# Kernel tuning notes

Measured on AMD Instinct MI355X. Metric: run time of the kernel, lower is better.

The kernel has to match this reference:

```python
import jax, jax.numpy as jnp
import numpy as np

# dims (see shape_source): emb_dim=256, input_size=256 -> d_model=1024
B, L = 8, 1024
QUES = 4000
EMB = 256
DM = 1024          # input_size + 768
DI = 2048          # expand * d_model
N = 16             # d_state
DTR = 64           # dt_rank = ceil(d_model/16)
K = 4              # d_conv
EPS = 1e-12


def setup_inputs() -> dict:
    key = jax.random.key(0)
    ks = jax.random.split(key, 16)
    s = 0.02
    nrm = lambda k, sh: jax.random.normal(k, sh, dtype=jnp.float32) * s
    return {
        "x": jax.random.randint(ks[0], (B, L), 0, 2 * QUES + 1),
        "q_id": jax.random.randint(ks[1], (B, L), 0, QUES),
        "emb_table": nrm(ks[2], (2 * QUES + 1, EMB)),
        "ques_cont": nrm(ks[3], (QUES, 768)),
        "ln0_g": jnp.ones((DM,), jnp.float32),
        "ln0_b": jnp.zeros((DM,), jnp.float32),
        "in_proj_w": nrm(ks[4], (2 * DI, DM)),
        "conv_w": nrm(ks[5], (DI, K)),
        "conv_b": jnp.zeros((DI,), jnp.float32),
        "x_proj_w": nrm(ks[6], (DTR + 2 * N, DI)),
        "dt_proj_w": nrm(ks[7], (DI, DTR)),
        "dt_proj_b": nrm(ks[8], (DI,)),
        "A_log": jnp.log(jax.random.uniform(ks[9], (DI, N), jnp.float32, 1.0, 16.0)),
        "D_param": jnp.ones((DI,), jnp.float32),
        "out_proj_w": nrm(ks[10], (DM, DI)),
        "ln1_g": jnp.ones((DM,), jnp.float32),
        "ln1_b": jnp.zeros((DM,), jnp.float32),
        "fc_w": nrm(ks[11], (QUES, DM)),
        "fc_b": jnp.zeros((QUES,), jnp.float32),
    }


def _ln(x, g, b):
    m = x.mean(-1, keepdims=True)
    v = ((x - m) ** 2).mean(-1, keepdims=True)
    return (x - m) / jnp.sqrt(v + EPS) * g + b


def _mamba(xm, in_proj_w, conv_w, conv_b, x_proj_w, dt_proj_w, dt_proj_b,
           A_log, D_param, out_proj_w):
    # xm: [B, L, DM]
    u_r = xm @ in_proj_w.T                           # [B, L, 2*DI]
    u, r = jnp.split(u_r, 2, axis=-1)                # each [B, L, DI]
    Lq = u.shape[1]
    # causal depthwise conv1d (padding=K-1, truncated to L)
    u_pad = jnp.pad(u, ((0, 0), (K - 1, 0), (0, 0)))
    conv = sum(u_pad[:, k:k + Lq, :] * conv_w[:, k] for k in range(K)) + conv_b
    u = jax.nn.silu(conv)
    dbl = u @ x_proj_w.T                             # [B, L, DTR+2N]
    dt, Bm, Cm = dbl[..., :DTR], dbl[..., DTR:DTR + N], dbl[..., DTR + N:]
    delta = jax.nn.softplus(dt @ dt_proj_w.T + dt_proj_b)   # [B, L, DI]
    A = -jnp.exp(A_log)                              # [DI, N]

    def step(h, ins):
        d_t, b_t, c_t, u_t = ins                     # [B,DI],[B,N],[B,N],[B,DI]
        dA = jnp.exp(d_t[:, :, None] * A)            # [B, DI, N]
        h = dA * h + d_t[:, :, None] * b_t[:, None, :] * u_t[:, :, None]
        y_t = jnp.einsum('bdn,bn->bd', h, c_t)
        return h, y_t

    xs = (delta.transpose(1, 0, 2), Bm.transpose(1, 0, 2),
          Cm.transpose(1, 0, 2), u.transpose(1, 0, 2))
    h0 = jnp.zeros((u.shape[0], DI, N), u.dtype)
    _, ys = jax.lax.scan(step, h0, xs)               # ys: [L, B, DI]
    y = ys.transpose(1, 0, 2) + u * D_param
    y = y * jax.nn.silu(r)
    return y @ out_proj_w.T                          # [B, L, DM]


def reference(x, q_id, emb_table, ques_cont, ln0_g, ln0_b, in_proj_w, conv_w,
              conv_b, x_proj_w, dt_proj_w, dt_proj_b, A_log, D_param,
              out_proj_w, ln1_g, ln1_b, fc_w, fc_b):
    x_e = emb_table[x]                               # [B, L, 256]
    x_c = ques_cont[q_id]                            # [B, L, 768]
    item = _ln(jnp.concatenate([x_e, x_c], axis=-1), ln0_g, ln0_b)
    # source loop applies every layer to item_emb; only the last layer's
    # output is used, so compute exactly that one layer (num_layers=2 branch).
    h = _mamba(item, in_proj_w, conv_w, conv_b, x_proj_w, dt_proj_w,
               dt_proj_b, A_log, D_param, out_proj_w)
    out = _ln(h + item, ln1_g, ln1_b)
    return jax.nn.sigmoid(out @ fc_w.T + fc_b)       # [B, L, QUES]
```

## Files before the change

kernel.cpp:

```cpp
#include <hip/hip_runtime.h>
#include <cstdint>
#include <cstddef>

#define L_SEQ 1024
#define BATCH 8
#define DMODEL 1024
#define DINNER 2048
#define NSTATE 16
#define DTRANK 64
#define NQ 4000
#define NROWS (BATCH * L_SEQ)
#define CH 32
#define NCH (L_SEQ / CH)

typedef float f32x4 __attribute__((ext_vector_type(4)));
typedef __bf16 bf16x8 __attribute__((ext_vector_type(8)));

#define AS1 __attribute__((address_space(1)))
#define AS3 __attribute__((address_space(3)))

__device__ __forceinline__ unsigned short f2bf(float f) {
  union { float f; unsigned int u; } c; c.f = f;
  unsigned int u = c.u;
  unsigned int r = u + 0x7fffu + ((u >> 16) & 1u);
  return (unsigned short)(r >> 16);
}

__device__ __forceinline__ float sigmoidf_(float x) { return 1.f / (1.f + expf(-x)); }

__global__ void cast_bf16_k(const float* __restrict__ src, unsigned short* __restrict__ dst, int n) {
  int i = blockIdx.x * blockDim.x + threadIdx.x;
  if (i < n) dst[i] = f2bf(src[i]);
}

__device__ __forceinline__ float blk_sum(float v, float* s) {
  #pragma unroll
  for (int o = 32; o > 0; o >>= 1) v += __shfl_down(v, o, 64);
  int w = threadIdx.x >> 6;
  if ((threadIdx.x & 63) == 0) s[w] = v;
  __syncthreads();
  float r = s[0] + s[1] + s[2] + s[3];
  __syncthreads();
  return r;
}

__global__ __launch_bounds__(256) void embed_ln0_k(
    const int* __restrict__ x, const int* __restrict__ qid,
    const float* __restrict__ emb, const float* __restrict__ qc,
    const float* __restrict__ g, const float* __restrict__ bta,
    float* __restrict__ item, unsigned short* __restrict__ item_bf)
{
  __shared__ float sbuf[4];
  int i = blockIdx.x;
  int t = threadIdx.x;
  float4 v;
  if (t < 64) v = *(const float4*)&emb[(size_t)x[i] * 256 + t * 4];
  else        v = *(const float4*)&qc[(size_t)qid[i] * 768 + t * 4 - 256];
  float tot = blk_sum(v.x + v.y + v.z + v.w, sbuf);
  float mean = tot * (1.f / 1024.f);
  float dx = v.x - mean, dy = v.y - mean, dz = v.z - mean, dw = v.w - mean;
  float var = blk_sum(dx*dx + dy*dy + dz*dz + dw*dw, sbuf) * (1.f / 1024.f);
  float rstd = rsqrtf(var + 1e-12f);
  float vals[4] = {dx, dy, dz, dw};
  size_t rb = (size_t)i * 1024;
  #pragma unroll
  for (int j = 0; j < 4; j++) {
    int c = t * 4 + j;
    float o = vals[j] * rstd * g[c] + bta[c];
    item[rb + c] = o;
    item_bf[rb + c] = f2bf(o);
  }
}

template <int EPI>
__global__ __launch_bounds__(256) void gemm_bt_k(
    const unsigned short* __restrict__ A, const unsigned short* __restrict__ Bw,
    float* __restrict__ C, const float* __restrict__ bias,
    unsigned short* __restrict__ aux,
    int M, int N, int K)
{
  __shared__ __align__(16) unsigned short As[128 * 64];
  __shared__ __align__(16) unsigned short Bs[128 * 64];
  const int tid = threadIdx.x;
  const int m0 = blockIdx.x * 128;
  const int n0 = blockIdx.y * 128;
  const int w = tid >> 6, lane = tid & 63;
  const int wrow = (w >> 1) * 64, wcol = (w & 1) * 64;
  const int quad = lane >> 4, lid = lane & 15;

  const int srow = lane >> 3;
  const int schunk = (lane & 7) ^ srow;

  const unsigned short* Abase = A + (size_t)(m0 + w * 8 + srow) * K + schunk * 8;
  const unsigned short* Bbase[4];
  #pragma unroll
  for (int i = 0; i < 4; i++) {
    int rB = n0 + w * 8 + i * 32 + srow;
    if (rB > N - 1) rB = N - 1;
    Bbase[i] = Bw + (size_t)rB * K + schunk * 8;
  }

  f32x4 acc[4][4] = {};

  for (int k0 = 0; k0 < K; k0 += 64) {
    #pragma unroll
    for (int i = 0; i < 4; i++) {
      int rA = w * 8 + i * 32;
      __builtin_amdgcn_global_load_lds(
          (const AS1 unsigned int*)(Abase + (size_t)i * 32 * K + k0),
          (AS3 unsigned int*)&As[rA * 64], 16, 0, 0);
      __builtin_amdgcn_global_load_lds(
          (const AS1 unsigned int*)(Bbase[i] + k0),
          (AS3 unsigned int*)&Bs[rA * 64], 16, 0, 0);
    }
    __syncthreads();
    #pragma unroll
    for (int kk = 0; kk < 64; kk += 32) {
      bf16x8 af[4], bfr[4];
      #pragma unroll
      for (int mi = 0; mi < 4; mi++) {
        int r = wrow + mi * 16 + lid;
        int slot = ((kk >> 3) + quad) ^ (lid & 7);
        af[mi] = *(const bf16x8*)&As[r * 64 + slot * 8];
      }
      #pragma unroll
      for (int ni = 0; ni < 4; ni++) {
        int r = wcol + ni * 16 + lid;
        int slot = ((kk >> 3) + quad) ^ (lid & 7);
        bfr[ni] = *(const bf16x8*)&Bs[r * 64 + slot * 8];
      }
      #pragma unroll
      for (int mi = 0; mi < 4; mi++)
        #pragma unroll
        for (int ni = 0; ni < 4; ni++)
          acc[mi][ni] = __builtin_amdgcn_mfma_f32_16x16x32_bf16(af[mi], bfr[ni], acc[mi][ni], 0, 0, 0);
    }
    __syncthreads();
  }

  #pragma unroll
  for (int mi = 0; mi < 4; mi++) {
    #pragma unroll
    for (int ni = 0; ni < 4; ni++) {
      int col = n0 + wcol + ni * 16 + lid;
      if (col >= N) continue;
      #pragma unroll
      for (int r = 0; r < 4; r++) {
        int row = m0 + wrow + mi * 16 + quad * 4 + r;
        float v = acc[mi][ni][r];
        if (EPI == 1) v = sigmoidf_(v + bias[col]);
        if (EPI == 2) { float xx = v + bias[col]; v = fmaxf(xx, 0.f) + log1pf(expf(-fabsf(xx))); }
        C[(size_t)row * N + col] = v;
        if (EPI == 3 && col < 64) aux[(size_t)row * 64 + col] = f2bf(v);
      }
    }
  }
}

template <int EPI>
__global__ __launch_bounds__(512, 2) void gemm256_k(
    const unsigned short* __restrict__ A, const unsigned short* __restrict__ Bw,
    float* __restrict__ C, const float* __restrict__ bias,
    int M, int N, int K)
{
  __shared__ __align__(16) unsigned short As[2][256 * 64];
  __shared__ __align__(16) unsigned short Bs[2][256 * 64];
  const int tid = threadIdx.x;

  const int gx = gridDim.x;
  const int nwg = gx * gridDim.y;
  int bid = blockIdx.y * gx + blockIdx.x;
  if ((nwg & 7) == 0) bid = (bid & 7) * (nwg >> 3) + (bid >> 3);
  const int m0 = (bid % gx) * 256;
  const int n0 = (bid / gx) * 256;

  const int w = tid >> 6, lane = tid & 63;
  const int wrow = (w >> 2) * 128;
  const int wcol = (w & 3) * 64;
  const int quad = lane >> 4, lid = lane & 15;

  const int srow = lane >> 3;
  const int schunk = (lane & 7) ^ srow;

  const unsigned short* Ab = A + (size_t)(m0 + w * 8 + srow) * K + schunk * 8;
  const unsigned short* Bb[4];
  #pragma unroll
  for (int i = 0; i < 4; i++) {
    int rB = n0 + w * 8 + i * 64 + srow;
    if (rB > N - 1) rB = N - 1;
    Bb[i] = Bw + (size_t)rB * K + schunk * 8;
  }

  f32x4 acc[8][4] = {};

  auto stage = [&](int buf, int k0) {
    #pragma unroll
    for (int i = 0; i < 4; i++) {
      int rg = (i * 64 + w * 8) * 64;
      __builtin_amdgcn_global_load_lds(
          (const AS1 unsigned int*)(Ab + (size_t)i * 64 * K + k0),
          (AS3 unsigned int*)&As[buf][rg], 16, 0, 0);
      __builtin_amdgcn_global_load_lds(
          (const AS1 unsigned int*)(Bb[i] + k0),
          (AS3 unsigned int*)&Bs[buf][rg], 16, 0, 0);
    }
  };

  const int nt = K >> 6;
  stage(0, 0);
  __syncthreads();

  for (int kt = 0; kt < nt; ++kt) {
    const int cur = kt & 1;
    if (kt + 1 < nt) stage(cur ^ 1, (kt + 1) << 6);

    bf16x8 bfr[4][2];
    #pragma unroll
    for (int ni = 0; ni < 4; ni++) {
      #pragma unroll
      for (int kk2 = 0; kk2 < 2; kk2++) {
        int r = wcol + ni * 16 + lid;
        int slot = (kk2 * 4 + quad) ^ (lid & 7);
        bfr[ni][kk2] = *(const bf16x8*)&Bs[cur][r * 64 + slot * 8];
      }
    }
    #pragma unroll
    for (int mi = 0; mi < 8; mi++) {
      bf16x8 af[2];
      #pragma unroll
      for (int kk2 = 0; kk2 < 2; kk2++) {
        int r = wrow + mi * 16 + lid;
        int slot = (kk2 * 4 + quad) ^ (lid & 7);
        af[kk2] = *(const bf16x8*)&As[cur][r * 64 + slot * 8];
      }
      #pragma unroll
      for (int ni = 0; ni < 4; ni++) {
        acc[mi][ni] = __builtin_amdgcn_mfma_f32_16x16x32_bf16(af[0], bfr[ni][0], acc[mi][ni], 0, 0, 0);
        acc[mi][ni] = __builtin_amdgcn_mfma_f32_16x16x32_bf16(af[1], bfr[ni][1], acc[mi][ni], 0, 0, 0);
      }
    }
    __syncthreads();
  }

  #pragma unroll
  for (int mi = 0; mi < 8; mi++) {
    #pragma unroll
    for (int ni = 0; ni < 4; ni++) {
      int col = n0 + wcol + ni * 16 + lid;
      if (col >= N) continue;
      #pragma unroll
      for (int r = 0; r < 4; r++) {
        int row = m0 + wrow + mi * 16 + quad * 4 + r;
        float v = acc[mi][ni][r];
        if (EPI == 1) v = sigmoidf_(v + bias[col]);
        C[(size_t)row * N + col] = v;
      }
    }
  }
}

__global__ void conv_silu_k(const float* __restrict__ u_r, const float* __restrict__ w,
                            const float* __restrict__ cb, float* __restrict__ uc,
                            unsigned short* __restrict__ uc_bf)
{
  int idx = blockIdx.x * blockDim.x + threadIdx.x;
  if (idx >= BATCH * L_SEQ * DINNER) return;
  int d = idx & (DINNER - 1);
  int l = (idx >> 11) & (L_SEQ - 1);
  int b = idx >> 21;
  float4 wv = ((const float4*)w)[d];
  size_t rb = ((size_t)b * L_SEQ + l) * (2 * DINNER) + d;
  float acc = cb[d];
  acc += wv.w * u_r[rb];
  if (l >= 1) acc += wv.z * u_r[rb - (2 * DINNER)];
  if (l >= 2) acc += wv.y * u_r[rb - 2 * (2 * DINNER)];
  if (l >= 3) acc += wv.x * u_r[rb - 3 * (2 * DINNER)];
  float s = acc * sigmoidf_(acc);
  uc[idx] = s;
  uc_bf[idx] = f2bf(s);
}

__global__ void a2_k(const float* __restrict__ Alog, float* __restrict__ a2t)
{
  int i = blockIdx.x * blockDim.x + threadIdx.x;
  if (i >= DINNER * NSTATE) return;
  int d = i >> 4, n = i & 15;
  a2t[n * DINNER + d] = -expf(Alog[i]) * 1.4426950408889634f;
}

__global__ __launch_bounds__(64) void scan1_k(
    const float* __restrict__ dlt, const float* __restrict__ uc,
    const float* __restrict__ dbl, const float* __restrict__ a2t,
    float* __restrict__ Pbuf, float* __restrict__ Qbuf)
{
  int c = blockIdx.x;
  int dg = blockIdx.y;
  int b = blockIdx.z;
  int d = dg * 64 + threadIdx.x;
  float a2[NSTATE], P[NSTATE], q[NSTATE];
  #pragma unroll
  for (int n = 0; n < NSTATE; n++) {
    a2[n] = a2t[n * DINNER + d];
    P[n] = 1.f; q[n] = 0.f;
  }
  size_t base = ((size_t)(b * L_SEQ + c * CH)) * DINNER + d;
  const float* bc = dbl + (size_t)(b * L_SEQ + c * CH) * 96 + 64;
  for (int t = 0; t < CH; t++) {
    float dl = dlt[base];
    float du = dl * uc[base];
    #pragma unroll
    for (int n = 0; n < NSTATE; n++) {
      float dA = exp2f(dl * a2[n]);
      q[n] = dA * q[n] + du * bc[n];
      P[n] *= dA;
    }
    base += DINNER;
    bc += 96;
  }
  size_t ob = ((size_t)((b * NCH + c) * NSTATE)) * DINNER + d;
  #pragma unroll
  for (int n = 0; n < NSTATE; n++) {
    Pbuf[ob + (size_t)n * DINNER] = P[n];
    Qbuf[ob + (size_t)n * DINNER] = q[n];
  }
}

__global__ void scan_carry_k(const float* __restrict__ Pbuf, float* __restrict__ Qbuf)
{
  int idx = blockIdx.x * blockDim.x + threadIdx.x;
  if (idx >= BATCH * NSTATE * DINNER) return;
  int d = idx & (DINNER - 1);
  int n = (idx >> 11) & 15;
  int b = idx >> 15;
  float h = 0.f;
  for (int c = 0; c < NCH; c++) {
    size_t o = ((size_t)((b * NCH + c) * NSTATE + n)) * DINNER + d;
    float P = Pbuf[o];
    float q = Qbuf[o];
    Qbuf[o] = h;
    h = P * h + q;
  }
}

__global__ __launch_bounds__(64) void scan2_k(
    const float* __restrict__ dlt, const float* __restrict__ uc,
    const float* __restrict__ dbl, const float* __restrict__ a2t,
    const float* __restrict__ Qbuf, const float* __restrict__ u_r,
    const float* __restrict__ Dp, unsigned short* __restrict__ ybf)
{
  int c = blockIdx.x;
  int dg = blockIdx.y;
  int b = blockIdx.z;
  int d = dg * 64 + threadIdx.x;
  float a2[NSTATE], h[NSTATE];
  size_t ob = ((size_t)((b * NCH + c) * NSTATE)) * DINNER + d;
  #pragma unroll
  for (int n = 0; n < NSTATE; n++) {
    a2[n] = a2t[n * DINNER + d];
    h[n] = Qbuf[ob + (size_t)n * DINNER];
  }
  float Dd = Dp[d];
  size_t base = ((size_t)(b * L_SEQ + c * CH)) * DINNER + d;
  const float* bc = dbl + (size_t)(b * L_SEQ + c * CH) * 96 + 64;
  const float* rp = u_r + (size_t)(b * L_SEQ + c * CH) * (2 * DINNER) + DINNER + d;
  for (int t = 0; t < CH; t++) {
    float dl = dlt[base];
    float uval = uc[base];
    float du = dl * uval;
    float yv = 0.f;
    #pragma unroll
    for (int n = 0; n < NSTATE; n++) {
      float dA = exp2f(dl * a2[n]);
      h[n] = dA * h[n] + du * bc[n];
      yv += h[n] * bc[NSTATE + n];
    }
    float rv = *rp;
    float val = (yv + uval * Dd) * (rv * sigmoidf_(rv));
    ybf[base] = f2bf(val);
    base += DINNER;
    bc += 96;
    rp += 2 * DINNER;
  }
}

__global__ __launch_bounds__(256) void ln1_k(
    const float* __restrict__ mamba, const float* __restrict__ item,
    const float* __restrict__ g, const float* __restrict__ bta,
    unsigned short* __restrict__ out_bf)
{
  __shared__ float sbuf[4];
  int i = blockIdx.x;
  int t = threadIdx.x;
  size_t rb = (size_t)i * 1024 + t * 4;
  float4 v = *(const float4*)&mamba[rb];
  float4 w4 = *(const float4*)&item[rb];
  v.x += w4.x; v.y += w4.y; v.z += w4.z; v.w += w4.w;
  float tot = blk_sum(v.x + v.y + v.z + v.w, sbuf);
  float mean = tot * (1.f / 1024.f);
  float dx = v.x - mean, dy = v.y - mean, dz = v.z - mean, dw = v.w - mean;
  float var = blk_sum(dx*dx + dy*dy + dz*dz + dw*dw, sbuf) * (1.f / 1024.f);
  float rstd = rsqrtf(var + 1e-12f);
  float vals[4] = {dx, dy, dz, dw};
  #pragma unroll
  for (int j = 0; j < 4; j++) {
    int c = t * 4 + j;
    out_bf[(size_t)i * 1024 + c] = f2bf(vals[j] * rstd * g[c] + bta[c]);
  }
}

extern "C" void kernel_launch(void* const* d_in, const int* in_sizes, int n_in,
                              void* d_out, int out_size, void* d_ws, size_t ws_size,
                              hipStream_t stream)
{
  (void)in_sizes; (void)n_in; (void)out_size; (void)ws_size;
  const int*   x     = (const int*)d_in[0];
  const int*   qid   = (const int*)d_in[1];
  const float* emb   = (const float*)d_in[2];
  const float* qc    = (const float*)d_in[3];
  const float* ln0g  = (const float*)d_in[4];
  const float* ln0b  = (const float*)d_in[5];
  const float* w_in  = (const float*)d_in[6];
  const float* convw = (const float*)d_in[7];
  const float* convb = (const float*)d_in[8];
  const float* w_x   = (const float*)d_in[9];
  const float* w_dt  = (const float*)d_in[10];
  const float* dtb   = (const float*)d_in[11];
  const float* Alog  = (const float*)d_in[12];
  const float* Dp    = (const float*)d_in[13];
  const float* w_out = (const float*)d_in[14];
  const float* ln1g  = (const float*)d_in[15];
  const float* ln1b  = (const float*)d_in[16];
  const float* w_fc  = (const float*)d_in[17];
  const float* fcb   = (const float*)d_in[18];
  float* out = (float*)d_out;

  char* base = (char*)d_ws;
  size_t off = 0;
  auto carve = [&](size_t bytes) -> char* {
    char* p = base + off;
    off = (off + bytes + 255) & ~(size_t)255;
    return p;
  };
  float* item  = (float*)carve((size_t)NROWS * 1024 * 4);
  float* u_r   = (float*)carve((size_t)NROWS * 4096 * 4);
  float* uc    = (float*)carve((size_t)NROWS * 2048 * 4);
  float* dbl   = (float*)carve((size_t)NROWS * 96 * 4);
  float* dlt   = (float*)carve((size_t)NROWS * 2048 * 4);
  float* mamba = (float*)carve((size_t)NROWS * 1024 * 4);
  unsigned short* bfbuf  = (unsigned short*)carve((size_t)NROWS * 2048 * 2);
  unsigned short* bw_in  = (unsigned short*)carve((size_t)4096 * 1024 * 2);
  unsigned short* bw_x   = (unsigned short*)carve((size_t)96 * 2048 * 2);
  unsigned short* bw_dt  = (unsigned short*)carve((size_t)2048 * 64 * 2);
  unsigned short* bw_out = (unsigned short*)carve((size_t)1024 * 2048 * 2);
  unsigned short* bw_fc  = (unsigned short*)carve((size_t)4000 * 1024 * 2);
  float* a2t   = (float*)carve((size_t)DINNER * NSTATE * 4);

  unsigned short* dt_bf = (unsigned short*)mamba;
  float* Pbuf = mamba;
  float* Qbuf = (float*)bfbuf;
  unsigned short* y_bf = (unsigned short*)mamba;
  float* mamba_out = u_r;

  auto cv = [&](const float* s, unsigned short* dst, int n) {
    cast_bf16_k<<<(n + 255) / 256, 256, 0, stream>>>(s, dst, n);
  };
  cv(w_in,  bw_in,  4096 * 1024);
  cv(w_x,   bw_x,   96 * 2048);
  cv(w_dt,  bw_dt,  2048 * 64);
  cv(w_out, bw_out, 1024 * 2048);
  cv(w_fc,  bw_fc,  4000 * 1024);
  a2_k<<<(DINNER * NSTATE + 255) / 256, 256, 0, stream>>>(Alog, a2t);

  embed_ln0_k<<<NROWS, 256, 0, stream>>>(x, qid, emb, qc, ln0g, ln0b, item, bfbuf);

  gemm256_k<0><<<dim3(32, 16), 512, 0, stream>>>(bfbuf, bw_in, u_r, nullptr, NROWS, 4096, 1024);

  conv_silu_k<<<(NROWS * DINNER) / 256, 256, 0, stream>>>(u_r, convw, convb, uc, bfbuf);

  gemm_bt_k<3><<<dim3(64, 1), 256, 0, stream>>>(bfbuf, bw_x, dbl, nullptr, dt_bf, NROWS, 96, 2048);

  gemm_bt_k<2><<<dim3(64, 16), 256, 0, stream>>>(dt_bf, bw_dt, dlt, dtb, nullptr, NROWS, 2048, 64);

  scan1_k<<<dim3(NCH, 32, BATCH), 64, 0, stream>>>(dlt, uc, dbl, a2t, Pbuf, Qbuf);
  scan_carry_k<<<(BATCH * NSTATE * DINNER) / 256, 256, 0, stream>>>(Pbuf, Qbuf);
  scan2_k<<<dim3(NCH, 32, BATCH), 64, 0, stream>>>(dlt, uc, dbl, a2t, Qbuf, u_r, Dp, y_bf);

  gemm_bt_k<0><<<dim3(64, 8), 256, 0, stream>>>(y_bf, bw_out, mamba_out, nullptr, nullptr, NROWS, 1024, 2048);

  ln1_k<<<NROWS, 256, 0, stream>>>(mamba_out, item, ln1g, ln1b, bfbuf);

  gemm256_k<1><<<dim3(32, 16), 512, 0, stream>>>(bfbuf, bw_fc, out, fcb, NROWS, 4000, 1024);
}
```

Before: 861.5 us.

## Split-K x_proj GEMM, drop 256-tile GEMM, double scan chunk size

Replaces the single-column-block x_proj GEMM (64 workgroups) with a 4-way split-K kernel that writes partial slabs, plus a reduction kernel that sums them and emits the bf16 dt operand. This is meant to expose more parallelism on a GEMM with narrow N. It also removes the double-buffered 256x256 GEMM and runs in_proj and fc on the simpler 128x128 kernel. The scan chunk length goes from 32 to 64, which halves the number of chunks but gives each thread a longer serial loop. The extra slab round trip through memory and the loss of the larger tile's reuse and prefetching are the costs.

```diff
diff --git a/kernel.cpp b/kernel.cpp
--- a/kernel.cpp
+++ b/kernel.cpp
@@ -10,8 +10,9 @@
 #define DTRANK 64
 #define NQ 4000
 #define NROWS (BATCH * L_SEQ)
-#define CH 32
+#define CH 64
 #define NCH (L_SEQ / CH)
+#define XKN 96
 
 typedef float f32x4 __attribute__((ext_vector_type(4)));
 typedef __bf16 bf16x8 __attribute__((ext_vector_type(8)));
@@ -76,7 +77,6 @@
 __global__ __launch_bounds__(256) void gemm_bt_k(
     const unsigned short* __restrict__ A, const unsigned short* __restrict__ Bw,
     float* __restrict__ C, const float* __restrict__ bias,
-    unsigned short* __restrict__ aux,
     int M, int N, int K)
 {
   __shared__ __align__(16) unsigned short As[128 * 64];
@@ -151,112 +151,101 @@
         if (EPI == 1) v = sigmoidf_(v + bias[col]);
         if (EPI == 2) { float xx = v + bias[col]; v = fmaxf(xx, 0.f) + log1pf(expf(-fabsf(xx))); }
         C[(size_t)row * N + col] = v;
-        if (EPI == 3 && col < 64) aux[(size_t)row * 64 + col] = f2bf(v);
-      }
-    }
-  }
-}
-
-template <int EPI>
-__global__ __launch_bounds__(512, 2) void gemm256_k(
+      }
+    }
+  }
+}
+
+__global__ __launch_bounds__(256) void gemm_xk_k(
     const unsigned short* __restrict__ A, const unsigned short* __restrict__ Bw,
-    float* __restrict__ C, const float* __restrict__ bias,
-    int M, int N, int K)
-{
-  __shared__ __align__(16) unsigned short As[2][256 * 64];
-  __shared__ __align__(16) unsigned short Bs[2][256 * 64];
+    float* __restrict__ slab, int M, int K, int KS)
+{
+  __shared__ __align__(16) unsigned short As[128 * 64];
+  __shared__ __align__(16) unsigned short Bs[128 * 64];
   const int tid = threadIdx.x;
-
-  const int gx = gridDim.x;
-  const int nwg = gx * gridDim.y;
-  int bid = blockIdx.y * gx + blockIdx.x;
-  if ((nwg & 7) == 0) bid = (bid & 7) * (nwg >> 3) + (bid >> 3);
-  const int m0 = (bid % gx) * 256;
-  const int n0 = (bid / gx) * 256;
-
+  const int m0 = blockIdx.x * 128;
+  const int kslice = blockIdx.y;
   const int w = tid >> 6, lane = tid & 63;
-  const int wrow = (w >> 2) * 128;
-  const int wcol = (w & 3) * 64;
+  const int wrow = (w >> 1) * 64, wcol = (w & 1) * 64;
   const int quad = lane >> 4, lid = lane & 15;
 
   const int srow = lane >> 3;
   const int schunk = (lane & 7) ^ srow;
 
-  const unsigned short* Ab = A + (size_t)(m0 + w * 8 + srow) * K + schunk * 8;
-  const unsigned short* Bb[4];
+  const unsigned short* Abase = A + (size_t)(m0 + w * 8 + srow) * K + schunk * 8;
+  const unsigned short* Bbase[4];
   #pragma unroll
   for (int i = 0; i < 4; i++) {
-    int rB = n0 + w * 8 + i * 64 + srow;
-    if (rB > N - 1) rB = N - 1;
-    Bb[i] = Bw + (size_t)rB * K + schunk * 8;
-  }
-
-  f32x4 acc[8][4] = {};
-
-  auto stage = [&](int buf, int k0) {
+    int rB = w * 8 + i * 32 + srow;
+    if (rB > XKN - 1) rB = XKN - 1;
+    Bbase[i] = Bw + (size_t)rB * K + schunk * 8;
+  }
+
+  f32x4 acc[4][4] = {};
+  const int kbeg = kslice * KS, kend = kbeg + KS;
+
+  for (int k0 = kbeg; k0 < kend; k0 += 64) {
     #pragma unroll
     for (int i = 0; i < 4; i++) {
-      int rg = (i * 64 + w * 8) * 64;
+      int rA = w * 8 + i * 32;
       __builtin_amdgcn_global_load_lds(
-          (const AS1 unsigned int*)(Ab + (size_t)i * 64 * K + k0),
-          (AS3 unsigned int*)&As[buf][rg], 16, 0, 0);
+          (const AS1 unsigned int*)(Abase + (size_t)i * 32 * K + k0),
+          (AS3 unsigned int*)&As[rA * 64], 16, 0, 0);
       __builtin_amdgcn_global_load_lds(
-          (const AS1 unsigned int*)(Bb[i] + k0),
-          (AS3 unsigned int*)&Bs[buf][rg], 16, 0, 0);
-    }
-  };
-
-  const int nt = K >> 6;
-  stage(0, 0);
-  __syncthreads();
-
-  for (int kt = 0; kt < nt; ++kt) {
-    const int cur = kt & 1;
-    if (kt + 1 < nt) stage(cur ^ 1, (kt + 1) << 6);
-
-    bf16x8 bfr[4][2];
+          (const AS1 unsigned int*)(Bbase[i] + k0),
+          (AS3 unsigned int*)&Bs[rA * 64], 16, 0, 0);
+    }
+    __syncthreads();
+    #pragma unroll
+    for (int kk = 0; kk < 64; kk += 32) {
+      bf16x8 af[4], bfr[4];
+      #pragma unroll
+      for (int mi = 0; mi < 4; mi++) {
+        int r = wrow + mi * 16 + lid;
+        int slot = ((kk >> 3) + quad) ^ (lid & 7);
+        af[mi] = *(const bf16x8*)&As[r * 64 + slot * 8];
+      }
+      #pragma unroll
+      for (int ni = 0; ni < 4; ni++) {
+        int r = wcol + ni * 16 + lid;
+        int slot = ((kk >> 3) + quad) ^ (lid & 7);
+        bfr[ni] = *(const bf16x8*)&Bs[r * 64 + slot * 8];
+      }
+      #pragma unroll
+      for (int mi = 0; mi < 4; mi++)
+        #pragma unroll
+        for (int ni = 0; ni < 4; ni++)
+          acc[mi][ni] = __builtin_amdgcn_mfma_f32_16x16x32_bf16(af[mi], bfr[ni], acc[mi][ni], 0, 0, 0);
+    }
+    __syncthreads();
+  }
+
+  float* Cs = slab + (size_t)kslice * M * XKN;
+  #pragma unroll
+  for (int mi = 0; mi < 4; mi++) {
     #pragma unroll
     for (int ni = 0; ni < 4; ni++) {
-      #pragma unroll
-      for (int kk2 = 0; kk2 < 2; kk2++) {
-        int r = wcol + ni * 16 + lid;
-        int slot = (kk2 * 4 + quad) ^ (lid & 7);
-        bfr[ni][kk2] = *(const bf16x8*)&Bs[cur][r * 64 + slot * 8];
-      }
-    }
-    #pragma unroll
-    for (int mi = 0; mi < 8; mi++) {
-      bf16x8 af[2];
-      #pragma unroll
-      for (int kk2 = 0; kk2 < 2; kk2++) {
-        int r = wrow + mi * 16 + lid;
-        int slot = (kk2 * 4 + quad) ^ (lid & 7);
-        af[kk2] = *(const bf16x8*)&As[cur][r * 64 + slot * 8];
-      }
-      #pragma unroll
-      for (int ni = 0; ni < 4; ni++) {
-        acc[mi][ni] = __builtin_amdgcn_mfma_f32_16x16x32_bf16(af[0], bfr[ni][0], acc[mi][ni], 0, 0, 0);
-        acc[mi][ni] = __builtin_amdgcn_mfma_f32_16x16x32_bf16(af[1], bfr[ni][1], acc[mi][ni], 0, 0, 0);
-      }
-    }
-    __syncthreads();
-  }
-
-  #pragma unroll
-  for (int mi = 0; mi < 8; mi++) {
-    #pragma unroll
-    for (int ni = 0; ni < 4; ni++) {
-      int col = n0 + wcol + ni * 16 + lid;
-      if (col >= N) continue;
+      int col = wcol + ni * 16 + lid;
+      if (col >= XKN) continue;
       #pragma unroll
       for (int r = 0; r < 4; r++) {
         int row = m0 + wrow + mi * 16 + quad * 4 + r;
-        float v = acc[mi][ni][r];
-        if (EPI == 1) v = sigmoidf_(v + bias[col]);
-        C[(size_t)row * N + col] = v;
-      }
-    }
-  }
+        Cs[(size_t)row * XKN + col] = acc[mi][ni][r];
+      }
+    }
+  }
+}
+
+__global__ void xproj_reduce_k(const float* __restrict__ slab, float* __restrict__ dbl,
+                               unsigned short* __restrict__ dt_bf)
+{
+  int i = blockIdx.x * blockDim.x + threadIdx.x;
+  if (i >= NROWS * XKN) return;
+  const size_t S = (size_t)NROWS * XKN;
+  float s = slab[i] + slab[i + S] + slab[i + 2 * S] + slab[i + 3 * S];
+  dbl[i] = s;
+  int row = i / XKN, col = i - row * XKN;
+  if (col < 64) dt_bf[(size_t)row * 64 + col] = f2bf(s);
 }
 
 __global__ void conv_silu_k(const float* __restrict__ u_r, const float* __restrict__ w,
@@ -304,7 +293,7 @@
     P[n] = 1.f; q[n] = 0.f;
   }
   size_t base = ((size_t)(b * L_SEQ + c * CH)) * DINNER + d;
-  const float* bc = dbl + (size_t)(b * L_SEQ + c * CH) * 96 + 64;
+  const float* bc = dbl + (size_t)(b * L_SEQ + c * CH) * XKN + 64;
   for (int t = 0; t < CH; t++) {
     float dl = dlt[base];
     float du = dl * uc[base];
@@ -315,7 +304,7 @@
       P[n] *= dA;
     }
     base += DINNER;
-    bc += 96;
+    bc += XKN;
   }
   size_t ob = ((size_t)((b * NCH + c) * NSTATE)) * DINNER + d;
   #pragma unroll
@@ -361,7 +350,7 @@
   }
   float Dd = Dp[d];
   size_t base = ((size_t)(b * L_SEQ + c * CH)) * DINNER + d;
-  const float* bc = dbl + (size_t)(b * L_SEQ + c * CH) * 96 + 64;
+  const float* bc = dbl + (size_t)(b * L_SEQ + c * CH) * XKN + 64;
   const float* rp = u_r + (size_t)(b * L_SEQ + c * CH) * (2 * DINNER) + DINNER + d;
   for (int t = 0; t < CH; t++) {
     float dl = dlt[base];
@@ -378,7 +367,7 @@
     float val = (yv + uval * Dd) * (rv * sigmoidf_(rv));
     ybf[base] = f2bf(val);
     base += DINNER;
-    bc += 96;
+    bc += XKN;
     rp += 2 * DINNER;
   }
 }
@@ -444,17 +433,18 @@
   float* item  = (float*)carve((size_t)NROWS * 1024 * 4);
   float* u_r   = (float*)carve((size_t)NROWS * 4096 * 4);
   float* uc    = (float*)carve((size_t)NROWS * 2048 * 4);
-  float* dbl   = (float*)carve((size_t)NROWS * 96 * 4);
+  float* dbl   = (float*)carve((size_t)NROWS * XKN * 4);
   float* dlt   = (float*)carve((size_t)NROWS * 2048 * 4);
   float* mamba = (float*)carve((size_t)NROWS * 1024 * 4);
   unsigned short* bfbuf  = (unsigned short*)carve((size_t)NROWS * 2048 * 2);
   unsigned short* bw_in  = (unsigned short*)carve((size_t)4096 * 1024 * 2);
-  unsigned short* bw_x   = (unsigned short*)carve((size_t)96 * 2048 * 2);
+  unsigned short* bw_x   = (unsigned short*)carve((size_t)XKN * 2048 * 2);
   unsigned short* bw_dt  = (unsigned short*)carve((size_t)2048 * 64 * 2);
   unsigned short* bw_out = (unsigned short*)carve((size_t)1024 * 2048 * 2);
   unsigned short* bw_fc  = (unsigned short*)carve((size_t)4000 * 1024 * 2);
   float* a2t   = (float*)carve((size_t)DINNER * NSTATE * 4);
 
+  float* slab = dlt;
   unsigned short* dt_bf = (unsigned short*)mamba;
   float* Pbuf = mamba;
   float* Qbuf = (float*)bfbuf;
@@ -465,7 +455,7 @@
     cast_bf16_k<<<(n + 255) / 256, 256, 0, stream>>>(s, dst, n);
   };
   cv(w_in,  bw_in,  4096 * 1024);
-  cv(w_x,   bw_x,   96 * 2048);
+  cv(w_x,   bw_x,   XKN * 2048);
   cv(w_dt,  bw_dt,  2048 * 64);
   cv(w_out, bw_out, 1024 * 2048);
   cv(w_fc,  bw_fc,  4000 * 1024);
@@ -473,21 +463,22 @@
 
   embed_ln0_k<<<NROWS, 256, 0, stream>>>(x, qid, emb, qc, ln0g, ln0b, item, bfbuf);
 
-  gemm256_k<0><<<dim3(32, 16), 512, 0, stream>>>(bfbuf, bw_in, u_r, nullptr, NROWS, 4096, 1024);
+  gemm_bt_k<0><<<dim3(64, 32), 256, 0, stream>>>(bfbuf, bw_in, u_r, nullptr, NROWS, 4096, 1024);
 
   conv_silu_k<<<(NROWS * DINNER) / 256, 256, 0, stream>>>(u_r, convw, convb, uc, bfbuf);
 
-  gemm_bt_k<3><<<dim3(64, 1), 256, 0, stream>>>(bfbuf, bw_x, dbl, nullptr, dt_bf, NROWS, 96, 2048);
-
-  gemm_bt_k<2><<<dim3(64, 16), 256, 0, stream>>>(dt_bf, bw_dt, dlt, dtb, nullptr, NROWS, 2048, 64);
+  gemm_xk_k<<<dim3(64, 4), 256, 0, stream>>>(bfbuf, bw_x, slab, NROWS, 2048, 512);
+  xproj_reduce_k<<<(NROWS * XKN) / 256, 256, 0, stream>>>(slab, dbl, dt_bf);
+
+  gemm_bt_k<2><<<dim3(64, 16), 256, 0, stream>>>(dt_bf, bw_dt, dlt, dtb, NROWS, 2048, 64);
 
   scan1_k<<<dim3(NCH, 32, BATCH), 64, 0, stream>>>(dlt, uc, dbl, a2t, Pbuf, Qbuf);
   scan_carry_k<<<(BATCH * NSTATE * DINNER) / 256, 256, 0, stream>>>(Pbuf, Qbuf);
   scan2_k<<<dim3(NCH, 32, BATCH), 64, 0, stream>>>(dlt, uc, dbl, a2t, Qbuf, u_r, Dp, y_bf);
 
-  gemm_bt_k<0><<<dim3(64, 8), 256, 0, stream>>>(y_bf, bw_out, mamba_out, nullptr, nullptr, NROWS, 1024, 2048);
+  gemm_bt_k<0><<<dim3(64, 8), 256, 0, stream>>>(y_bf, bw_out, mamba_out, nullptr, NROWS, 1024, 2048);
 
   ln1_k<<<NROWS, 256, 0, stream>>>(mamba_out, item, ln1g, ln1b, bfbuf);
 
-  gemm256_k<1><<<dim3(32, 16), 512, 0, stream>>>(bfbuf, bw_fc, out, fcb, NROWS, 4000, 1024);
-}
+  gemm_bt_k<1><<<dim3(64, 32), 256, 0, stream>>>(bfbuf, bw_fc, out, fcb, NROWS, 4000, 1024);
+}
```

New measurement: 855.3 us. No clear change (-0.7%).
